# Kernel tuning notes

Hardware: AMD Instinct MI355X
Metric: run time of the kernel (lower is better)

## Reference

```python
import jax, jax.numpy as jnp
import numpy as np
from jax.experimental.ode import odeint

DT = 0.01  # matches init kwarg dt


def setup_inputs() -> dict:
    key = jax.random.key(0)
    kx, kw = jax.random.split(key)
    B, D, T = 8192, 128, 64
    x = jax.random.normal(kx, (B, D), dtype=jnp.float32)
    # nnx.Linear kernel (in_features, out_features), lecun-normal-like scale
    W = jax.random.normal(kw, (D, D), dtype=jnp.float32) / np.float32(np.sqrt(D))
    return {"x": x, "W": W, "T": T}


def reference(x, W, T):
    # dynamics_fn(z, t) = Linear(z) = z @ W  (no bias), time-invariant linear ODE
    time_points = DT * jnp.arange(1, T + 1, dtype=jnp.float32)  # dt*[1..T]
    # odeint: y0 = x is the state at time_points[0]; preds: (T, B, D)
    preds = odeint(lambda z, t: z @ W, x, time_points)
    return jnp.transpose(preds, (1, 0, 2))  # (B, T, D)
```

## Files before the change

### kernel.cpp

```cpp
#include <hip/hip_runtime.h>
#include <stdint.h>

#define DD   128
#define TT   64
#define BB   8192
#define NPOW 12

typedef float  f32x4  __attribute__((ext_vector_type(4)));
typedef __bf16 bf16x8 __attribute__((ext_vector_type(8)));

__device__ __forceinline__ unsigned short f2bf(float f) {
  unsigned u = __builtin_bit_cast(unsigned, f);
  u += 0x7fffu + ((u >> 16) & 1u);
  return (unsigned short)(u >> 16);
}

__device__ __forceinline__ void async_load16(const void* g, void* l) {
  __builtin_amdgcn_global_load_lds(
      (const __attribute__((address_space(1))) unsigned int*)g,
      (__attribute__((address_space(3))) unsigned int*)l,
      16, 0, 0);
}

__global__ void cvt_x_kernel(const float* __restrict__ x, unsigned short* __restrict__ xb) {
  int i = (blockIdx.x * 256 + threadIdx.x) * 4;
  float4 v = *(const float4*)(x + i);
  unsigned long long u =  (unsigned long long)f2bf(v.x)
                       | ((unsigned long long)f2bf(v.y) << 16)
                       | ((unsigned long long)f2bf(v.z) << 32)
                       | ((unsigned long long)f2bf(v.w) << 48);
  *(unsigned long long*)(xb + i) = u;
}

__global__ void powmm_kernel(const float* __restrict__ W, float* __restrict__ Wp,
                             int aPow, int bBase, int dstBase) {
  int mat = blockIdx.x >> 3;
  int rb  = blockIdx.x & 7;
  int bPow = bBase + mat;
  const float* A = (aPow == 1) ? W : (Wp + (aPow - 2) * DD * DD);
  const float* B = (bPow == 1) ? W : (Wp + (bPow - 2) * DD * DD);
  float* C = Wp + (dstBase + mat - 2) * DD * DD;

  __shared__ float Bs[DD * DD];
  __shared__ float As[16 * DD];
  for (int i = threadIdx.x; i < DD * DD; i += 256) Bs[i] = B[i];
  for (int i = threadIdx.x; i < 16 * DD; i += 256) As[i] = A[rb * 16 * DD + i];
  __syncthreads();

  int r  = threadIdx.x >> 4;
  int c0 = (threadIdx.x & 15) * 8;
  float acc[8] = {0.f, 0.f, 0.f, 0.f, 0.f, 0.f, 0.f, 0.f};
  for (int k = 0; k < DD; ++k) {
    float a = As[r * DD + k];
#pragma unroll
    for (int jj = 0; jj < 8; ++jj) acc[jj] += a * Bs[k * DD + c0 + jj];
  }
  int gr = rb * 16 + r;
#pragma unroll
  for (int jj = 0; jj < 8; ++jj) C[gr * DD + c0 + jj] = acc[jj];
}

__global__ void combine_kernel(const float* __restrict__ W, const float* __restrict__ Wp,
                               unsigned short* __restrict__ Pb) {
  int j = blockIdx.x;
  double t = (double)j * 0.01;
  float c[NPOW + 1];
  double cc = 1.0;
  for (int n = 1; n <= NPOW; ++n) { cc *= t / (double)n; c[n] = (float)cc; }

  for (int o = threadIdx.x; o < DD * DD; o += 256) {
    int d = o >> 7;
    int k = o & 127;
    float acc = (k == d) ? 1.0f : 0.0f;
    acc += c[1] * W[k * DD + d];
#pragma unroll
    for (int n = 2; n <= NPOW; ++n) acc += c[n] * Wp[(n - 2) * DD * DD + k * DD + d];
    Pb[j * DD * DD + o] = f2bf(acc);
  }
}

__global__ __launch_bounds__(256) void gemm_kernel(
    const unsigned short* __restrict__ xb,
    const unsigned short* __restrict__ Pb,
    float* __restrict__ out) {
  __shared__ __attribute__((aligned(16))) unsigned short Al[DD * DD];
  __shared__ __attribute__((aligned(16))) unsigned short Bl[DD * DD];

  const int bt   = blockIdx.x;
  const int j    = blockIdx.y;
  const int tid  = threadIdx.x;
  const int w    = tid >> 6;
  const int l    = tid & 63;
  const int quad = l >> 4;
  const int li   = l & 15;

  const unsigned short* gA = xb + bt * DD * DD;
  const unsigned short* gB = Pb + j * DD * DD;

#pragma unroll
  for (int i = 0; i < 8; ++i) {
    int ci  = i * 4 + w;
    int row = ci * 4 + quad;
    int cc  = li ^ (row & 15);
    async_load16(gA + row * DD + cc * 8, (void*)(Al + ci * 512));
    async_load16(gB + row * DD + cc * 8, (void*)(Bl + ci * 512));
  }
  __syncthreads();

  const int mq = (w >> 1) * 64;
  const int nq = (w & 1) * 64;

  f32x4 acc[4][4];
#pragma unroll
  for (int mt = 0; mt < 4; ++mt)
#pragma unroll
    for (int nt = 0; nt < 4; ++nt) acc[mt][nt] = (f32x4){0.f, 0.f, 0.f, 0.f};

#pragma unroll
  for (int ks = 0; ks < 4; ++ks) {
    bf16x8 af[4], bf[4];
#pragma unroll
    for (int mt = 0; mt < 4; ++mt) {
      int row = mq + mt * 16 + li;
      int sc  = (ks * 4 + quad) ^ (row & 15);
      af[mt] = *(const bf16x8*)(Al + row * DD + sc * 8);
    }
#pragma unroll
    for (int nt = 0; nt < 4; ++nt) {
      int row = nq + nt * 16 + li;
      int sc  = (ks * 4 + quad) ^ (row & 15);
      bf[nt] = *(const bf16x8*)(Bl + row * DD + sc * 8);
    }
#pragma unroll
    for (int mt = 0; mt < 4; ++mt)
#pragma unroll
      for (int nt = 0; nt < 4; ++nt)
        acc[mt][nt] = __builtin_amdgcn_mfma_f32_16x16x32_bf16(af[mt], bf[nt], acc[mt][nt], 0, 0, 0);
  }

  float* o = out + (size_t)(bt * DD) * (TT * DD) + j * DD;
#pragma unroll
  for (int mt = 0; mt < 4; ++mt) {
#pragma unroll
    for (int nt = 0; nt < 4; ++nt) {
      int col = nq + nt * 16 + li;
#pragma unroll
      for (int r = 0; r < 4; ++r) {
        int row = mq + mt * 16 + quad * 4 + r;
        o[(size_t)row * (TT * DD) + col] = acc[mt][nt][r];
      }
    }
  }
}

extern "C" void kernel_launch(void* const* d_in, const int* in_sizes, int n_in,
                              void* d_out, int out_size, void* d_ws, size_t ws_size,
                              hipStream_t stream) {
  const float* x = (const float*)d_in[0];
  const float* W = (const float*)d_in[1];
  float* out = (float*)d_out;

  float* Wp = (float*)d_ws;
  unsigned short* Pb = (unsigned short*)((char*)d_ws + (NPOW - 1) * DD * DD * sizeof(float));
  unsigned short* xb = Pb + TT * DD * DD;

  cvt_x_kernel<<<BB * DD / (256 * 4), 256, 0, stream>>>(x, xb);

  powmm_kernel<<< 8, 256, 0, stream>>>(W, Wp, 1, 1, 2);
  powmm_kernel<<<16, 256, 0, stream>>>(W, Wp, 2, 1, 3);
  powmm_kernel<<<32, 256, 0, stream>>>(W, Wp, 4, 1, 5);
  powmm_kernel<<<32, 256, 0, stream>>>(W, Wp, 8, 1, 9);

  combine_kernel<<<TT, 256, 0, stream>>>(W, Wp, Pb);

  gemm_kernel<<<dim3(BB / DD, TT), 256, 0, stream>>>(xb, Pb, out);
}
```

Measured before the change: 401.5 us.

## Cut Taylor order, transpose W upfront, load GEMM operands directly from global

Reduces the Taylor series from 12 to 8 powers, which removes one power-matrix launch. W is transposed first so the combine step reads the power matrices contiguously with vectorized loads, and combine is spread over more blocks. The GEMM drops its LDS staging and reads bf16 fragments straight from global memory, relying on cache. Output writes become nontemporal stores. The lower series order risks accuracy at larger t, and reading from global without LDS may give less efficient access patterns.

```diff
diff --git a/kernel.cpp b/kernel.cpp
--- a/kernel.cpp
+++ b/kernel.cpp
@@ -4,7 +4,7 @@
 #define DD   128
 #define TT   64
 #define BB   8192
-#define NPOW 12
+#define NPOW 8
 
 typedef float  f32x4  __attribute__((ext_vector_type(4)));
 typedef __bf16 bf16x8 __attribute__((ext_vector_type(8)));
@@ -13,13 +13,6 @@
   unsigned u = __builtin_bit_cast(unsigned, f);
   u += 0x7fffu + ((u >> 16) & 1u);
   return (unsigned short)(u >> 16);
-}
-
-__device__ __forceinline__ void async_load16(const void* g, void* l) {
-  __builtin_amdgcn_global_load_lds(
-      (const __attribute__((address_space(1))) unsigned int*)g,
-      (__attribute__((address_space(3))) unsigned int*)l,
-      16, 0, 0);
 }
 
 __global__ void cvt_x_kernel(const float* __restrict__ x, unsigned short* __restrict__ xb) {
@@ -32,60 +25,76 @@
   *(unsigned long long*)(xb + i) = u;
 }
 
-__global__ void powmm_kernel(const float* __restrict__ W, float* __restrict__ Wp,
-                             int aPow, int bBase, int dstBase) {
-  int mat = blockIdx.x >> 3;
-  int rb  = blockIdx.x & 7;
-  int bPow = bBase + mat;
-  const float* A = (aPow == 1) ? W : (Wp + (aPow - 2) * DD * DD);
-  const float* B = (bPow == 1) ? W : (Wp + (bPow - 2) * DD * DD);
-  float* C = Wp + (dstBase + mat - 2) * DD * DD;
+__global__ void transpose_kernel(const float* __restrict__ W, float* __restrict__ Wt) {
+  __shared__ float t[32][33];
+  int bx = blockIdx.x & 3, by = blockIdx.x >> 2;
+  int r = threadIdx.x >> 3;
+  int c = (threadIdx.x & 7) * 4;
+  float4 v = *(const float4*)(W + (by * 32 + r) * DD + bx * 32 + c);
+  t[r][c] = v.x; t[r][c + 1] = v.y; t[r][c + 2] = v.z; t[r][c + 3] = v.w;
+  __syncthreads();
+  float4 o = { t[c + 0][r], t[c + 1][r], t[c + 2][r], t[c + 3][r] };
+  *(float4*)(Wt + (bx * 32 + r) * DD + by * 32 + c) = o;
+}
+
+__global__ __launch_bounds__(256) void powmm_kernel(float* __restrict__ Wp,
+                                                    int aPow, int bBase, int dstBase) {
+  int mat = blockIdx.x >> 4;
+  int rb  = blockIdx.x & 15;
+  const float* A = Wp + (aPow - 1) * DD * DD;
+  const float* B = Wp + (bBase + mat - 1) * DD * DD;
+  float* C = Wp + (dstBase + mat - 1) * DD * DD;
 
   __shared__ float Bs[DD * DD];
-  __shared__ float As[16 * DD];
-  for (int i = threadIdx.x; i < DD * DD; i += 256) Bs[i] = B[i];
-  for (int i = threadIdx.x; i < 16 * DD; i += 256) As[i] = A[rb * 16 * DD + i];
+  __shared__ float As[8 * DD];
+  for (int i = threadIdx.x; i < DD * DD / 4; i += 256)
+    ((float4*)Bs)[i] = ((const float4*)B)[i];
+  for (int i = threadIdx.x; i < 8 * DD / 4; i += 256)
+    ((float4*)As)[i] = ((const float4*)(A + rb * 8 * DD))[i];
   __syncthreads();
 
-  int r  = threadIdx.x >> 4;
-  int c0 = (threadIdx.x & 15) * 8;
-  float acc[8] = {0.f, 0.f, 0.f, 0.f, 0.f, 0.f, 0.f, 0.f};
+  int r  = threadIdx.x >> 5;
+  int c0 = (threadIdx.x & 31) * 4;
+  f32x4 acc = {0.f, 0.f, 0.f, 0.f};
   for (int k = 0; k < DD; ++k) {
     float a = As[r * DD + k];
-#pragma unroll
-    for (int jj = 0; jj < 8; ++jj) acc[jj] += a * Bs[k * DD + c0 + jj];
+    f32x4 b = *(const f32x4*)(Bs + k * DD + c0);
+    acc += a * b;
   }
-  int gr = rb * 16 + r;
-#pragma unroll
-  for (int jj = 0; jj < 8; ++jj) C[gr * DD + c0 + jj] = acc[jj];
+  *(f32x4*)(C + (rb * 8 + r) * DD + c0) = acc;
 }
 
-__global__ void combine_kernel(const float* __restrict__ W, const float* __restrict__ Wp,
-                               unsigned short* __restrict__ Pb) {
-  int j = blockIdx.x;
-  double t = (double)j * 0.01;
-  float c[NPOW + 1];
-  double cc = 1.0;
-  for (int n = 1; n <= NPOW; ++n) { cc *= t / (double)n; c[n] = (float)cc; }
+__global__ __launch_bounds__(256) void combine_kernel(const float* __restrict__ Wp,
+                                                      unsigned short* __restrict__ Pb) {
+  int j    = blockIdx.x >> 4;
+  int part = blockIdx.x & 15;
+  float c[NPOW];
+  double t = (double)j * 0.01, cc = 1.0;
+  for (int n = 1; n <= NPOW; ++n) { cc *= t / (double)n; c[n - 1] = (float)cc; }
 
-  for (int o = threadIdx.x; o < DD * DD; o += 256) {
-    int d = o >> 7;
-    int k = o & 127;
-    float acc = (k == d) ? 1.0f : 0.0f;
-    acc += c[1] * W[k * DD + d];
+  int e0 = part * 1024 + threadIdx.x * 4;
+  f32x4 acc;
 #pragma unroll
-    for (int n = 2; n <= NPOW; ++n) acc += c[n] * Wp[(n - 2) * DD * DD + k * DD + d];
-    Pb[j * DD * DD + o] = f2bf(acc);
+  for (int i = 0; i < 4; ++i) {
+    int e = e0 + i;
+    acc[i] = ((e >> 7) == (e & 127)) ? 1.0f : 0.0f;
   }
+#pragma unroll
+  for (int n = 0; n < NPOW; ++n) {
+    f32x4 w = *(const f32x4*)(Wp + n * DD * DD + e0);
+    acc += c[n] * w;
+  }
+  unsigned long long u =  (unsigned long long)f2bf(acc[0])
+                       | ((unsigned long long)f2bf(acc[1]) << 16)
+                       | ((unsigned long long)f2bf(acc[2]) << 32)
+                       | ((unsigned long long)f2bf(acc[3]) << 48);
+  *(unsigned long long*)(Pb + j * DD * DD + e0) = u;
 }
 
 __global__ __launch_bounds__(256) void gemm_kernel(
     const unsigned short* __restrict__ xb,
     const unsigned short* __restrict__ Pb,
     float* __restrict__ out) {
-  __shared__ __attribute__((aligned(16))) unsigned short Al[DD * DD];
-  __shared__ __attribute__((aligned(16))) unsigned short Bl[DD * DD];
-
   const int bt   = blockIdx.x;
   const int j    = blockIdx.y;
   const int tid  = threadIdx.x;
@@ -94,21 +103,11 @@
   const int quad = l >> 4;
   const int li   = l & 15;
 
+  const int mq = (w >> 1) * 64;
+  const int nq = (w & 1) * 64;
+
   const unsigned short* gA = xb + bt * DD * DD;
   const unsigned short* gB = Pb + j * DD * DD;
-
-#pragma unroll
-  for (int i = 0; i < 8; ++i) {
-    int ci  = i * 4 + w;
-    int row = ci * 4 + quad;
-    int cc  = li ^ (row & 15);
-    async_load16(gA + row * DD + cc * 8, (void*)(Al + ci * 512));
-    async_load16(gB + row * DD + cc * 8, (void*)(Bl + ci * 512));
-  }
-  __syncthreads();
-
-  const int mq = (w >> 1) * 64;
-  const int nq = (w & 1) * 64;
 
   f32x4 acc[4][4];
 #pragma unroll
@@ -120,17 +119,11 @@
   for (int ks = 0; ks < 4; ++ks) {
     bf16x8 af[4], bf[4];
 #pragma unroll
-    for (int mt = 0; mt < 4; ++mt) {
-      int row = mq + mt * 16 + li;
-      int sc  = (ks * 4 + quad) ^ (row & 15);
-      af[mt] = *(const bf16x8*)(Al + row * DD + sc * 8);
-    }
+    for (int mt = 0; mt < 4; ++mt)
+      af[mt] = *(const bf16x8*)(gA + (mq + mt * 16 + li) * DD + ks * 32 + quad * 8);
 #pragma unroll
-    for (int nt = 0; nt < 4; ++nt) {
-      int row = nq + nt * 16 + li;
-      int sc  = (ks * 4 + quad) ^ (row & 15);
-      bf[nt] = *(const bf16x8*)(Bl + row * DD + sc * 8);
-    }
+    for (int nt = 0; nt < 4; ++nt)
+      bf[nt] = *(const bf16x8*)(gB + (nq + nt * 16 + li) * DD + ks * 32 + quad * 8);
 #pragma unroll
     for (int mt = 0; mt < 4; ++mt)
 #pragma unroll
@@ -147,7 +140,7 @@
 #pragma unroll
       for (int r = 0; r < 4; ++r) {
         int row = mq + mt * 16 + quad * 4 + r;
-        o[(size_t)row * (TT * DD) + col] = acc[mt][nt][r];
+        __builtin_nontemporal_store(acc[mt][nt][r], &o[row * (TT * DD) + col]);
       }
     }
   }
@@ -161,17 +154,17 @@
   float* out = (float*)d_out;
 
   float* Wp = (float*)d_ws;
-  unsigned short* Pb = (unsigned short*)((char*)d_ws + (NPOW - 1) * DD * DD * sizeof(float));
+  unsigned short* Pb = (unsigned short*)((char*)d_ws + NPOW * DD * DD * sizeof(float));
   unsigned short* xb = Pb + TT * DD * DD;
 
   cvt_x_kernel<<<BB * DD / (256 * 4), 256, 0, stream>>>(x, xb);
+  transpose_kernel<<<16, 256, 0, stream>>>(W, Wp);
 
-  powmm_kernel<<< 8, 256, 0, stream>>>(W, Wp, 1, 1, 2);
-  powmm_kernel<<<16, 256, 0, stream>>>(W, Wp, 2, 1, 3);
-  powmm_kernel<<<32, 256, 0, stream>>>(W, Wp, 4, 1, 5);
-  powmm_kernel<<<32, 256, 0, stream>>>(W, Wp, 8, 1, 9);
+  powmm_kernel<<<16, 256, 0, stream>>>(Wp, 1, 1, 2);
+  powmm_kernel<<<32, 256, 0, stream>>>(Wp, 2, 1, 3);
+  powmm_kernel<<<64, 256, 0, stream>>>(Wp, 4, 1, 5);
 
-  combine_kernel<<<TT, 256, 0, stream>>>(W, Wp, Pb);
+  combine_kernel<<<TT * 16, 256, 0, stream>>>(Wp, Pb);
 
   gemm_kernel<<<dim3(BB / DD, TT), 256, 0, stream>>>(xb, Pb, out);
 }
```

New measurement: 344.4 us. 14.2% less time.
